# Performance work log

Hardware: AMD Instinct MI355X
Metric: run time of the kernel (lower is better)

The kernel has to match this reference:

```python
import jax, jax.numpy as jnp
import numpy as np

_MAX_SQRT_GRADIENT = 1000.0


@jax.custom_vjp
def sqrt_bound_derivative(x):
    return jnp.sqrt(x)

def _sbd_fwd(x):
    return jnp.sqrt(x), x

def _sbd_bwd(x, g):
    clipped_x4 = jnp.clip(4.0 * x, 1.0 / _MAX_SQRT_GRADIENT ** 2, None)
    return (g / jnp.sqrt(clipped_x4),)

sqrt_bound_derivative.defvjp(_sbd_fwd, _sbd_bwd)


def setup_inputs() -> dict:
    key = jax.random.key(0)
    ks = jax.random.split(key, 6)
    B, S, D, H = 4, 2048, 2560, 10
    bw = D // H  # 256
    activations = jax.random.normal(ks[0], (B, S, D), dtype=jnp.float32)
    position_ids = jnp.broadcast_to(jnp.arange(S, dtype=jnp.int64), (B, S))
    recurrent_param = jax.random.normal(ks[1], (D,), dtype=jnp.float32)
    input_gate_weight = jax.random.normal(ks[2], (H, bw, bw), dtype=jnp.float32) / np.sqrt(bw)
    input_gate_bias = jax.random.normal(ks[3], (H, bw), dtype=jnp.float32) * 0.1
    recurrent_gate_weight = jax.random.normal(ks[4], (H, bw, bw), dtype=jnp.float32) / np.sqrt(bw)
    recurrent_gate_bias = jax.random.normal(ks[5], (H, bw), dtype=jnp.float32) * 0.1
    return {
        "activations": activations,
        "position_ids": position_ids,
        "recurrent_param": recurrent_param,
        "input_gate_weight": input_gate_weight,
        "input_gate_bias": input_gate_bias,
        "recurrent_gate_weight": recurrent_gate_weight,
        "recurrent_gate_bias": recurrent_gate_bias,
    }


def _rglru(activations, position_ids, recurrent_param,
           input_gate_weight, input_gate_bias,
           recurrent_gate_weight, recurrent_gate_bias):
    B, S, D = activations.shape
    H, bw, _ = input_gate_weight.shape
    reset = (position_ids == 0)[:, :, None]  # [B, S, 1] bool

    x = activations.reshape(B, S, H, bw)
    # per-head gate projections (equivalent to torch baddbmm over heads)
    ig = jnp.einsum('bshi,hij->bshj', x, input_gate_weight) + input_gate_bias
    input_gate = jax.nn.sigmoid(ig.reshape(B, S, D))
    rg = jnp.einsum('bshi,hij->bshj', x, recurrent_gate_weight) + recurrent_gate_bias
    recurrent_gate = jax.nn.sigmoid(rg.reshape(B, S, D))

    log_a = -8.0 * recurrent_gate * jax.nn.softplus(recurrent_param)
    a = jnp.exp(log_a)                       # diagonal recurrence coeff
    a_square = jnp.exp(2.0 * log_a)

    gated_inputs = activations * input_gate
    multiplier = sqrt_bound_derivative(1.0 - a_square)
    multiplier = jnp.where(reset, 1.0, multiplier)
    normalized_x = gated_inputs * multiplier

    a = jnp.where(reset, 0.0, a)  # recurrent_gate * ~reset

    # linear scan over time in fp32 accumulation
    def step(h, inp):
        a_t, x_t = inp
        h = a_t * h + x_t
        return h, h

    h0 = jnp.zeros((B, D), dtype=jnp.float32)
    a_t = jnp.transpose(a, (1, 0, 2)).astype(jnp.float32)           # [S, B, D]
    x_t = jnp.transpose(normalized_x, (1, 0, 2)).astype(jnp.float32)
    _, ys = jax.lax.scan(step, h0, (a_t, x_t))
    return jnp.transpose(ys, (1, 0, 2)).astype(activations.dtype)


def reference(activations, position_ids, recurrent_param,
              input_gate_weight, input_gate_bias,
              recurrent_gate_weight, recurrent_gate_bias):
    return _rglru(activations, position_ids, recurrent_param,
                  input_gate_weight, input_gate_bias,
                  recurrent_gate_weight, recurrent_gate_bias)
```

## Files before the change

kernel.cpp:

```cpp
#include <hip/hip_runtime.h>
#include <hip/hip_bf16.h>

#define B_  4
#define S_  2048
#define D_  2560
#define H_  10
#define BW_ 256
#define NSUB 64
#define SUBL 32

typedef _Float16 f16;
typedef _Float16 f16x4 __attribute__((ext_vector_type(4)));
typedef _Float16 f16x8 __attribute__((ext_vector_type(8)));
typedef float    f32x4 __attribute__((ext_vector_type(4)));
typedef unsigned int uint32;

__global__ __launch_bounds__(256) void prep_kernel(
    const float* __restrict__ wig, const float* __restrict__ wrg,
    const float* __restrict__ rp,
    f16* __restrict__ wt_ig, f16* __restrict__ wt_rg, float* __restrict__ sp)
{
    __shared__ f16 tl[64 * 68];
    const int it = blockIdx.x, jt = blockIdx.y, h = blockIdx.z;
    const int tid = threadIdx.x;

    int flat = ((blockIdx.z * 4 + blockIdx.y) * 4 + blockIdx.x) * 256 + tid;
    if (flat < D_) {
        float x = rp[flat];
        sp[flat] = (x > 20.f) ? x : log1pf(__expf(x));
    }

    for (int m = 0; m < 2; m++) {
        const float* W = m ? wrg : wig;
        f16* WT = m ? wt_rg : wt_ig;
        if (m) __syncthreads();
        #pragma unroll
        for (int p = 0; p < 4; p++) {
            int idx = p * 256 + tid;
            int il = idx >> 4, j4 = (idx & 15) << 2;
            float4 v = *(const float4*)&W[(h << 16) + ((it * 64 + il) << 8)
                                          + jt * 64 + j4];
            f16x4 hv;
            hv[0] = (f16)v.x; hv[1] = (f16)v.y; hv[2] = (f16)v.z; hv[3] = (f16)v.w;
            *(f16x4*)&tl[il * 68 + j4] = hv;
        }
        __syncthreads();
        #pragma unroll
        for (int p = 0; p < 4; p++) {
            int idx = p * 256 + tid;
            int jl = idx >> 4, i4 = (idx & 15) << 2;
            f16x4 hv;
            hv[0] = tl[(i4 + 0) * 68 + jl];
            hv[1] = tl[(i4 + 1) * 68 + jl];
            hv[2] = tl[(i4 + 2) * 68 + jl];
            hv[3] = tl[(i4 + 3) * 68 + jl];
            *(f16x4*)&WT[(h << 16) + ((jt * 64 + jl) << 8) + it * 64 + i4] = hv;
        }
    }
}

__global__ __launch_bounds__(512, 4) void fused_kernel(
    const float* __restrict__ act,
    const f16* __restrict__ wt_ig, const f16* __restrict__ wt_rg,
    const float* __restrict__ big, const float* __restrict__ brg,
    const float* __restrict__ sp,
    float2* __restrict__ HP, uint32* __restrict__ packed)
{
    const int c = blockIdx.x;
    const int b = blockIdx.y, h = blockIdx.z;
    const int r0 = (b << 11) + (c << 6);
    const int tid = threadIdx.x;
    const int lane = tid & 63, w = tid >> 6;
    const int gate = w & 1;
    const int n0 = (w >> 1) * 64;
    const int l16 = lane & 15, lhi = lane >> 4;

    __shared__ f16 lds1[64 * 256];
    __shared__ f16 lds2[64 * 256];

    {
        const float* abase = act + (size_t)r0 * D_ + (h << 8);
        #pragma unroll
        for (int i = 0; i < 8; i++) {
            int f = i * 512 + tid;
            int row = f >> 6;
            int k4 = (f & 63) << 2;
            float4 v = *(const float4*)(abase + (size_t)row * D_ + k4);
            f16x4 hv;
            hv[0] = (f16)v.x; hv[1] = (f16)v.y; hv[2] = (f16)v.z; hv[3] = (f16)v.w;
            *(f16x4*)&lds1[row * 256 + (k4 ^ ((row & 7) << 3))] = hv;
        }
    }
    __syncthreads();

    const f16* wbase = (gate ? wt_rg : wt_ig) + (h << 16);
    f32x4 acc[4][4] = {};
    f16x8 ar[2][4], br[2][4];

    auto LDA = [&](int ks, f16x8* dst) {
        #pragma unroll
        for (int fm = 0; fm < 4; fm++) {
            int row = fm * 16 + l16;
            int k = ks * 32 + lhi * 8;
            dst[fm] = *(const f16x8*)&lds1[row * 256 + (k ^ ((row & 7) << 3))];
        }
    };
    auto LDB = [&](int ks, f16x8* dst) {
        int ka = ks * 32 + lhi * 8;
        #pragma unroll
        for (int fn = 0; fn < 4; fn++) {
            int j = n0 + fn * 16 + l16;
            dst[fn] = *(const f16x8*)(wbase + (j << 8) + ka);
        }
    };

    LDA(0, ar[0]); LDB(0, br[0]);
    #pragma unroll
    for (int ks = 0; ks < 8; ks++) {
        const int cur = ks & 1;
        if (ks < 7) { LDA(ks + 1, ar[cur ^ 1]); LDB(ks + 1, br[cur ^ 1]); }
        #pragma unroll
        for (int fm = 0; fm < 4; fm++)
        #pragma unroll
        for (int fn = 0; fn < 4; fn++)
            acc[fm][fn] = __builtin_amdgcn_mfma_f32_16x16x32_f16(
                ar[cur][fm], br[cur][fn], acc[fm][fn], 0, 0, 0);
    }
    __syncthreads();

    {
        const float* biasp = gate ? brg : big;
        #pragma unroll
        for (int fn = 0; fn < 4; fn++) {
            int coll = n0 + fn * 16 + l16;
            int dcol = (h << 8) + coll;
            float bias = biasp[dcol];
            float spv = sp[dcol];
            #pragma unroll
            for (int fm = 0; fm < 4; fm++)
            #pragma unroll
            for (int r = 0; r < 4; r++) {
                int rl = fm * 16 + lhi * 4 + r;
                int off = rl * 256 + (coll ^ ((rl & 7) << 3));
                float val = acc[fm][fn][r] + bias;
                float sig = 1.f / (1.f + __expf(-val));
                if (gate) lds2[off] = (f16)(-8.f * sig * spv);
                else      lds1[off] = (f16)((float)lds1[off] * sig);
            }
        }
    }
    __syncthreads();

    {
        const int sub = tid >> 8;
        const int col = tid & 255;
        const int s0 = sub << 5;
        const bool rst = (c == 0) && (sub == 0);
        uint32* op = packed + (size_t)(r0 + s0) * D_ + (h << 8) + col;
        float hacc = 0.f, P = 1.f;
        #pragma unroll 8
        for (int i = 0; i < 32; i++) {
            int s = s0 + i;
            int sw = col ^ ((s & 7) << 3);
            float xi = (float)lds1[s * 256 + sw];
            float la = (float)lds2[s * 256 + sw];
            float a = __expf(la);
            float mult;
            if (rst && i == 0) { a = 0.f; mult = 1.f; }
            else mult = sqrtf(fmaxf(fmaf(-a, a, 1.f), 0.f));
            hacc = fmaf(a, hacc, xi * mult);
            P *= a;
            union { uint32 u; f16 hh[2]; } cv;
            cv.hh[0] = (f16)hacc; cv.hh[1] = (f16)P;
            op[(size_t)i * D_] = cv.u;
        }
        const size_t o = ((size_t)((b * H_ + h) * NSUB) + (c * 2 + sub)) * 256 + col;
        HP[o] = make_float2(hacc, P);
    }
}

__global__ __launch_bounds__(256) void apply_kernel(
    const uint32* __restrict__ packed, const float2* __restrict__ HP,
    float* __restrict__ out)
{
    const int cc = blockIdx.x;
    const int b = blockIdx.y, h = blockIdx.z;
    const int col = threadIdx.x;
    const float2* hp = HP + (size_t)((b * H_ + h) * NSUB) * 256 + col;

    float cv = 0.f;
    int j = 0;
    for (; j + 8 <= cc; j += 8) {
        float2 v0 = hp[(j + 0) * 256], v1 = hp[(j + 1) * 256];
        float2 v2 = hp[(j + 2) * 256], v3 = hp[(j + 3) * 256];
        float2 v4 = hp[(j + 4) * 256], v5 = hp[(j + 5) * 256];
        float2 v6 = hp[(j + 6) * 256], v7 = hp[(j + 7) * 256];
        cv = fmaf(v0.y, cv, v0.x); cv = fmaf(v1.y, cv, v1.x);
        cv = fmaf(v2.y, cv, v2.x); cv = fmaf(v3.y, cv, v3.x);
        cv = fmaf(v4.y, cv, v4.x); cv = fmaf(v5.y, cv, v5.x);
        cv = fmaf(v6.y, cv, v6.x); cv = fmaf(v7.y, cv, v7.x);
    }
    for (; j < cc; j++) {
        float2 v = hp[j * 256];
        cv = fmaf(v.y, cv, v.x);
    }

    const int gr0 = (b << 11) + (cc << 5);
    const uint32* pp = packed + (size_t)gr0 * D_ + (h << 8) + col;
    float* op = out + (size_t)gr0 * D_ + (h << 8) + col;
    #pragma unroll 8
    for (int s = 0; s < SUBL; s++) {
        union { uint32 u; f16 hh[2]; } q;
        q.u = pp[(size_t)s * D_];
        op[(size_t)s * D_] = fmaf((float)q.hh[1], cv, (float)q.hh[0]);
    }
}

extern "C" void kernel_launch(void* const* d_in, const int* in_sizes, int n_in,
                              void* d_out, int out_size, void* d_ws, size_t ws_size,
                              hipStream_t stream)
{
    const float* act = (const float*)d_in[0];
    const float* rp  = (const float*)d_in[2];
    const float* wig = (const float*)d_in[3];
    const float* big = (const float*)d_in[4];
    const float* wrg = (const float*)d_in[5];
    const float* brg = (const float*)d_in[6];
    float* out = (float*)d_out;

    char* ws = (char*)d_ws;
    uint32* packed = (uint32*)ws;
    f16*   wt_ig = (f16*)(ws + (size_t)83886080);
    f16*   wt_rg = wt_ig + (size_t)H_ * BW_ * BW_;
    float* sp    = (float*)(wt_rg + (size_t)H_ * BW_ * BW_);
    float2* HP   = (float2*)(sp + D_);

    hipLaunchKernelGGL(prep_kernel, dim3(4, 4, H_), dim3(256),
                       0, stream, wig, wrg, rp, wt_ig, wt_rg, sp);
    hipLaunchKernelGGL(fused_kernel, dim3(32, B_, H_), dim3(512),
                       0, stream, act, wt_ig, wt_rg, big, brg, sp, HP, packed);
    hipLaunchKernelGGL(apply_kernel, dim3(NSUB, B_, H_), dim3(256),
                       0, stream, packed, HP, out);
}
```

Baseline: 263.2 us.

## Split fused kernel by column halves, add carry-scan kernel, flatten apply kernel

```diff
diff --git a/kernel.cpp b/kernel.cpp
--- a/kernel.cpp
+++ b/kernel.cpp
@@ -7,7 +7,7 @@
 #define H_  10
 #define BW_ 256
 #define NSUB 64
-#define SUBL 32
+#define NCH  (B_ * H_)
 
 typedef _Float16 f16;
 typedef _Float16 f16x4 __attribute__((ext_vector_type(4)));
@@ -59,36 +59,38 @@
     }
 }
 
-__global__ __launch_bounds__(512, 4) void fused_kernel(
+__global__ __launch_bounds__(256, 4) void fused_kernel(
     const float* __restrict__ act,
     const f16* __restrict__ wt_ig, const f16* __restrict__ wt_rg,
     const float* __restrict__ big, const float* __restrict__ brg,
     const float* __restrict__ sp,
     float2* __restrict__ HP, uint32* __restrict__ packed)
 {
-    const int c = blockIdx.x;
-    const int b = blockIdx.y, h = blockIdx.z;
+    const int g  = blockIdx.x;
+    const int ch = blockIdx.y;
+    const int h  = blockIdx.z;
+    const int b = g >> 5, c = g & 31;
     const int r0 = (b << 11) + (c << 6);
     const int tid = threadIdx.x;
-    const int lane = tid & 63, w = tid >> 6;
+    const int lane = tid & 63;
+    const int w = tid >> 6;
     const int gate = w & 1;
-    const int n0 = (w >> 1) * 64;
+    const int n0 = ch * 128 + (w >> 1) * 64;
     const int l16 = lane & 15, lhi = lane >> 4;
 
-    __shared__ f16 lds1[64 * 256];
-    __shared__ f16 lds2[64 * 256];
+    __shared__ f16 lds[64 * 256];
 
     {
         const float* abase = act + (size_t)r0 * D_ + (h << 8);
         #pragma unroll
-        for (int i = 0; i < 8; i++) {
-            int f = i * 512 + tid;
+        for (int i = 0; i < 16; i++) {
+            int f = i * 256 + tid;
             int row = f >> 6;
             int k4 = (f & 63) << 2;
             float4 v = *(const float4*)(abase + (size_t)row * D_ + k4);
             f16x4 hv;
             hv[0] = (f16)v.x; hv[1] = (f16)v.y; hv[2] = (f16)v.z; hv[3] = (f16)v.w;
-            *(f16x4*)&lds1[row * 256 + (k4 ^ ((row & 7) << 3))] = hv;
+            *(f16x4*)&lds[row * 256 + (k4 ^ ((row & 7) << 3))] = hv;
         }
     }
     __syncthreads();
@@ -102,7 +104,7 @@
         for (int fm = 0; fm < 4; fm++) {
             int row = fm * 16 + l16;
             int k = ks * 32 + lhi * 8;
-            dst[fm] = *(const f16x8*)&lds1[row * 256 + (k ^ ((row & 7) << 3))];
+            dst[fm] = *(const f16x8*)&lds[row * 256 + (k ^ ((row & 7) << 3))];
         }
     };
     auto LDB = [&](int ks, f16x8* dst) {
@@ -130,10 +132,11 @@
 
     {
         const float* biasp = gate ? brg : big;
+        const int halfoff = gate ? 128 : 0;
         #pragma unroll
         for (int fn = 0; fn < 4; fn++) {
-            int coll = n0 + fn * 16 + l16;
-            int dcol = (h << 8) + coll;
+            int coll = (w >> 1) * 64 + fn * 16 + l16;
+            int dcol = (h << 8) + ch * 128 + coll;
             float bias = biasp[dcol];
             float spv = sp[dcol];
             #pragma unroll
@@ -141,78 +144,89 @@
             #pragma unroll
             for (int r = 0; r < 4; r++) {
                 int rl = fm * 16 + lhi * 4 + r;
-                int off = rl * 256 + (coll ^ ((rl & 7) << 3));
                 float val = acc[fm][fn][r] + bias;
                 float sig = 1.f / (1.f + __expf(-val));
-                if (gate) lds2[off] = (f16)(-8.f * sig * spv);
-                else      lds1[off] = (f16)((float)lds1[off] * sig);
+                f16 ov = gate ? (f16)(-8.f * sig * spv) : (f16)sig;
+                lds[rl * 256 + halfoff + (coll ^ ((rl & 7) << 3))] = ov;
             }
         }
     }
     __syncthreads();
 
     {
-        const int sub = tid >> 8;
-        const int col = tid & 255;
+        const int sub = tid >> 7;
+        const int col = tid & 127;
         const int s0 = sub << 5;
-        const bool rst = (c == 0) && (sub == 0);
-        uint32* op = packed + (size_t)(r0 + s0) * D_ + (h << 8) + col;
+        const bool rst0 = (c == 0) && (sub == 0);
+        const float* ap = act + (size_t)(r0 + s0) * D_ + (h << 8) + ch * 128 + col;
+        uint32* op = packed + (size_t)(r0 + s0) * D_ + (h << 8) + ch * 128 + col;
         float hacc = 0.f, P = 1.f;
         #pragma unroll 8
         for (int i = 0; i < 32; i++) {
             int s = s0 + i;
             int sw = col ^ ((s & 7) << 3);
-            float xi = (float)lds1[s * 256 + sw];
-            float la = (float)lds2[s * 256 + sw];
+            float ig = (float)lds[s * 256 + sw];
+            float la = (float)lds[s * 256 + 128 + sw];
             float a = __expf(la);
+            float xv = ap[(size_t)i * D_];
             float mult;
-            if (rst && i == 0) { a = 0.f; mult = 1.f; }
+            if (rst0 && i == 0) { a = 0.f; mult = 1.f; }
             else mult = sqrtf(fmaxf(fmaf(-a, a, 1.f), 0.f));
-            hacc = fmaf(a, hacc, xi * mult);
+            hacc = fmaf(a, hacc, xv * ig * mult);
             P *= a;
             union { uint32 u; f16 hh[2]; } cv;
             cv.hh[0] = (f16)hacc; cv.hh[1] = (f16)P;
             op[(size_t)i * D_] = cv.u;
         }
-        const size_t o = ((size_t)((b * H_ + h) * NSUB) + (c * 2 + sub)) * 256 + col;
+        const size_t o = ((size_t)((b * H_ + h) * NSUB) + (c * 2 + sub)) * 256
+                         + ch * 128 + col;
         HP[o] = make_float2(hacc, P);
     }
 }
 
+__global__ __launch_bounds__(256) void carry_kernel(
+    const float2* __restrict__ HP, float* __restrict__ carry)
+{
+    const int chain = blockIdx.x;
+    const int col = threadIdx.x;
+    const float2* hp = HP + (size_t)chain * NSUB * 256 + col;
+    float* cp = carry + (size_t)chain * NSUB * 256 + col;
+    float cv = 0.f;
+    for (int l0 = 0; l0 < NSUB; l0 += 16) {
+        float2 v[16];
+        #pragma unroll
+        for (int j = 0; j < 16; j++) v[j] = hp[(l0 + j) * 256];
+        #pragma unroll
+        for (int j = 0; j < 16; j++) {
+            cp[(l0 + j) * 256] = cv;
+            cv = fmaf(v[j].y, cv, v[j].x);
+        }
+    }
+}
+
 __global__ __launch_bounds__(256) void apply_kernel(
-    const uint32* __restrict__ packed, const float2* __restrict__ HP,
+    const uint32* __restrict__ packed, const float* __restrict__ carry,
     float* __restrict__ out)
 {
-    const int cc = blockIdx.x;
-    const int b = blockIdx.y, h = blockIdx.z;
-    const int col = threadIdx.x;
-    const float2* hp = HP + (size_t)((b * H_ + h) * NSUB) * 256 + col;
-
-    float cv = 0.f;
-    int j = 0;
-    for (; j + 8 <= cc; j += 8) {
-        float2 v0 = hp[(j + 0) * 256], v1 = hp[(j + 1) * 256];
-        float2 v2 = hp[(j + 2) * 256], v3 = hp[(j + 3) * 256];
-        float2 v4 = hp[(j + 4) * 256], v5 = hp[(j + 5) * 256];
-        float2 v6 = hp[(j + 6) * 256], v7 = hp[(j + 7) * 256];
-        cv = fmaf(v0.y, cv, v0.x); cv = fmaf(v1.y, cv, v1.x);
-        cv = fmaf(v2.y, cv, v2.x); cv = fmaf(v3.y, cv, v3.x);
-        cv = fmaf(v4.y, cv, v4.x); cv = fmaf(v5.y, cv, v5.x);
-        cv = fmaf(v6.y, cv, v6.x); cv = fmaf(v7.y, cv, v7.x);
-    }
-    for (; j < cc; j++) {
-        float2 v = hp[j * 256];
-        cv = fmaf(v.y, cv, v.x);
-    }
-
-    const int gr0 = (b << 11) + (cc << 5);
-    const uint32* pp = packed + (size_t)gr0 * D_ + (h << 8) + col;
-    float* op = out + (size_t)gr0 * D_ + (h << 8) + col;
-    #pragma unroll 8
-    for (int s = 0; s < SUBL; s++) {
+    const uint32 n4 = (uint32)(B_ * S_ * D_) / 4;
+    uint32 i4 = blockIdx.x * 256 + threadIdx.x;
+    const uint32 stride = gridDim.x * 256;
+    for (; i4 < n4; i4 += stride) {
+        uint32 row = i4 / 640;
+        uint32 d = (i4 - row * 640) * 4;
+        uint32 b = row >> 11, s = row & (S_ - 1);
+        uint32 h = d >> 8, col = d & 255;
+        uint32 l = s >> 5;
+        const float4 cv = *(const float4*)
+            &carry[(((b * H_ + h) * NSUB + l) << 8) + col];
+        uint4 p = ((const uint4*)packed)[i4];
         union { uint32 u; f16 hh[2]; } q;
-        q.u = pp[(size_t)s * D_];
-        op[(size_t)s * D_] = fmaf((float)q.hh[1], cv, (float)q.hh[0]);
+        float4 o;
+        q.u = p.x; o.x = fmaf((float)q.hh[1], cv.x, (float)q.hh[0]);
+        q.u = p.y; o.y = fmaf((float)q.hh[1], cv.y, (float)q.hh[0]);
+        q.u = p.z; o.z = fmaf((float)q.hh[1], cv.z, (float)q.hh[0]);
+        q.u = p.w; o.w = fmaf((float)q.hh[1], cv.w, (float)q.hh[0]);
+        ((float4*)out)[i4] = o;
     }
 }
 
@@ -234,11 +248,14 @@
     f16*   wt_rg = wt_ig + (size_t)H_ * BW_ * BW_;
     float* sp    = (float*)(wt_rg + (size_t)H_ * BW_ * BW_);
     float2* HP   = (float2*)(sp + D_);
+    float* carry = (float*)wt_ig;
 
     hipLaunchKernelGGL(prep_kernel, dim3(4, 4, H_), dim3(256),
                        0, stream, wig, wrg, rp, wt_ig, wt_rg, sp);
-    hipLaunchKernelGGL(fused_kernel, dim3(32, B_, H_), dim3(512),
+    hipLaunchKernelGGL(fused_kernel, dim3(128, 2, H_), dim3(256),
                        0, stream, act, wt_ig, wt_rg, big, brg, sp, HP, packed);
-    hipLaunchKernelGGL(apply_kernel, dim3(NSUB, B_, H_), dim3(256),
-                       0, stream, packed, HP, out);
-}
+    hipLaunchKernelGGL(carry_kernel, dim3(NCH), dim3(256),
+                       0, stream, HP, carry);
+    hipLaunchKernelGGL(apply_kernel, dim3(2048), dim3(256),
+                       0, stream, packed, carry, out);
+}
```

Result: faster. 254.1 us (-3.4%).
